# Kernel optimization log

Hardware: AMD Instinct MI355X
Metric: run time of the kernel (lower is better)

Reference implementation:

```python
import jax, jax.numpy as jnp
import numpy as np

B, T, D, F, E = 2, 2048, 1024, 4096, 8
TOP_K = 2


def setup_inputs() -> dict:
    key = jax.random.key(0)
    k0, k1, k2, k3 = jax.random.split(key, 4)
    x = jax.random.normal(k0, (B, T, D), dtype=jnp.float32)
    Wr = jax.random.normal(k1, (D, E), dtype=jnp.float32) * 0.02   # router (no bias)
    W1 = jax.random.normal(k2, (E, D, F), dtype=jnp.float32) * 0.02
    b1 = jnp.zeros((E, F), dtype=jnp.float32)
    W2 = jax.random.normal(k3, (E, F, D), dtype=jnp.float32) * 0.02
    b2 = jnp.zeros((E, D), dtype=jnp.float32)
    return {"x": x, "Wr": Wr, "W1": W1, "b1": b1, "W2": W2, "b2": b2}


def reference(x, Wr, W1, b1, W2, b2):
    # Router: softmax over experts, top-k select, renormalize selected probs.
    logits = jnp.einsum('btd,de->bte', x, Wr)                      # [B,T,E]
    probs = jax.nn.softmax(logits, axis=-1)
    top_v, top_i = jax.lax.top_k(probs, TOP_K)                     # [B,T,K]
    top_v = top_v / jnp.sum(top_v, axis=-1, keepdims=True)
    # Combine weights: scatter renormalized top-k probs back to expert slots.
    combine = jnp.sum(jax.nn.one_hot(top_i, E, dtype=x.dtype) * top_v[..., None], axis=-2)  # [B,T,E]
    # Expert FFNs (Linear -> exact GELU -> Linear); dropout inactive at eval.
    h = jax.nn.gelu(jnp.einsum('btd,edf->ebtf', x, W1) + b1[:, None, None, :],
                    approximate=False)                              # [E,B,T,F]
    y = jnp.einsum('ebtf,efd->ebtd', h, W2) + b2[:, None, None, :]  # [E,B,T,D]
    # Weighted sum over selected experts (combine is zero for unselected).
    out = jnp.einsum('ebtd,bte->btd', y, combine)
    return out
```

## Files before the change

### kernel.cpp

```cpp
#include <hip/hip_runtime.h>
#include <hip/hip_bf16.h>
#include <math.h>

#define B_  2
#define T_  2048
#define D_  1024
#define F_  4096
#define E_  8
#define NTOK 4096
#define TOPK 2
#define NROW 8192

typedef unsigned short bf16_t;
typedef float f32x4 __attribute__((ext_vector_type(4)));
typedef int   i32x4 __attribute__((ext_vector_type(4)));

#define OFF_CNT   0
#define OFF_BASE  32
#define OFF_TIDX  64
#define OFF_TW    32832
#define OFF_LIST  65600
#define OFF_WGT   196672
#define OFF_H_OLD 327744
#define WS_OLD    (OFF_H_OLD + (size_t)NROW * F_ * 2)
#define OFF_SLOT  327744
#define OFF_XB    (1u << 20)
#define OFF_W1T   (OFF_XB  + (size_t)NTOK * D_ * 2)
#define OFF_W2T   (OFF_W1T + (size_t)E_ * F_ * D_ * 2)
#define OFF_HN    (OFF_W2T + (size_t)E_ * D_ * F_ * 2)
#define OFF_Y     (OFF_HN  + (size_t)NROW * F_ * 2)
#define WS_MFMA   (OFF_Y   + (size_t)NROW * D_ * 4)

__device__ __forceinline__ float gelu_exact(float v) {
    return 0.5f * v * (1.0f + erff(v * 0.70710678118654752440f));
}

__device__ __forceinline__ unsigned short f2bf_rne(float f) {
    union { float f; unsigned int u; } v; v.f = f;
    unsigned int r = (v.u + 0x7fffu + ((v.u >> 16) & 1u)) >> 16;
    return (unsigned short)r;
}

__device__ __forceinline__ float bf2f(unsigned int u) {
    union { unsigned int i; float f; } v; v.i = u << 16; return v.f;
}

__device__ __forceinline__ void gld16(const void* g, void* l) {
    __builtin_amdgcn_global_load_lds(
        (const __attribute__((address_space(1))) unsigned int*)g,
        (__attribute__((address_space(3))) unsigned int*)l, 16, 0, 0);
}

__device__ __forceinline__ void mfma16(const i32x4& a, const i32x4& b, f32x4& c) {
    asm("v_mfma_f32_16x16x32_bf16 %0, %1, %2, %0" : "+v"(c) : "v"(a), "v"(b));
}

__global__ __launch_bounds__(64) void router_kernel(
    const float* __restrict__ x, const float* __restrict__ Wr,
    int* __restrict__ top_idx, float* __restrict__ top_w,
    int* __restrict__ cnt, int* __restrict__ list, float* __restrict__ wgt,
    int* __restrict__ slot, int mode)
{
    const int n = blockIdx.x;
    const int lane = threadIdx.x;
    const float* xr = x + (size_t)n * D_;

    float acc[E_];
#pragma unroll
    for (int e = 0; e < E_; ++e) acc[e] = 0.f;

    for (int d = lane; d < D_; d += 64) {
        const float xv = xr[d];
#pragma unroll
        for (int e = 0; e < E_; ++e)
            acc[e] += xv * Wr[d * E_ + e];
    }
#pragma unroll
    for (int e = 0; e < E_; ++e) {
        float v = acc[e];
#pragma unroll
        for (int off = 32; off > 0; off >>= 1)
            v += __shfl_down(v, off, 64);
        acc[e] = v;
    }
    if (lane == 0) {
        float m = acc[0];
#pragma unroll
        for (int e = 1; e < E_; ++e) m = fmaxf(m, acc[e]);
        float p[E_];
#pragma unroll
        for (int e = 0; e < E_; ++e) p[e] = __expf(acc[e] - m);
        int i0 = 0; float v0 = p[0];
#pragma unroll
        for (int e = 1; e < E_; ++e) if (p[e] > v0) { v0 = p[e]; i0 = e; }
        int i1 = (i0 == 0) ? 1 : 0; float v1 = p[i1];
#pragma unroll
        for (int e = 0; e < E_; ++e) {
            if (e == i0) continue;
            if (p[e] > v1) { v1 = p[e]; i1 = e; }
        }
        const float inv = 1.f / (v0 + v1);
        const float w0 = v0 * inv, w1 = v1 * inv;
        top_idx[n * TOPK + 0] = i0;
        top_idx[n * TOPK + 1] = i1;
        top_w[n * TOPK + 0] = w0;
        top_w[n * TOPK + 1] = w1;
        if (mode & 1) {
            int p0 = atomicAdd(&cnt[i0], 1);
            list[i0 * NTOK + p0] = n;  wgt[i0 * NTOK + p0] = w0;
            int p1 = atomicAdd(&cnt[i1], 1);
            list[i1 * NTOK + p1] = n;  wgt[i1 * NTOK + p1] = w1;
            if (mode & 2) {
                slot[n * TOPK + 0] = (i0 << 16) | p0;
                slot[n * TOPK + 1] = (i1 << 16) | p1;
            }
        }
    }
}

__global__ void prefix_kernel(const int* __restrict__ cnt, int* __restrict__ base)
{
    if (threadIdx.x == 0 && blockIdx.x == 0) {
        int s = 0;
#pragma unroll
        for (int e = 0; e < E_; ++e) { base[e] = s; s += cnt[e]; }
    }
}

__global__ __launch_bounds__(256) void convert_x_kernel(
    const float* __restrict__ x, bf16_t* __restrict__ xb)
{
    const int i = blockIdx.x * 256 + threadIdx.x;
    const float4 v = ((const float4*)x)[i];
    uint2 o;
    o.x = (unsigned int)f2bf_rne(v.x) | ((unsigned int)f2bf_rne(v.y) << 16);
    o.y = (unsigned int)f2bf_rne(v.z) | ((unsigned int)f2bf_rne(v.w) << 16);
    ((uint2*)xb)[i] = o;
}

__global__ __launch_bounds__(256) void transpose_kernel(
    const float* __restrict__ src, bf16_t* __restrict__ dst, int R, int C)
{
    __shared__ float tile[64][65];
    const int z  = blockIdx.z;
    const int r0 = blockIdx.y * 64;
    const int c0 = blockIdx.x * 64;
    const float* s = src + (size_t)z * R * C;
    bf16_t*      d = dst + (size_t)z * R * C;
    const int tx = threadIdx.x & 63;
    const int ty = threadIdx.x >> 6;
#pragma unroll
    for (int i = 0; i < 16; ++i) {
        const int r = i * 4 + ty;
        tile[r][tx] = s[(size_t)(r0 + r) * C + c0 + tx];
    }
    __syncthreads();
#pragma unroll
    for (int i = 0; i < 16; ++i) {
        const int c = i * 4 + ty;
        d[(size_t)(c0 + c) * R + r0 + tx] = f2bf_rne(tile[tx][c]);
    }
}

__global__ __launch_bounds__(256) void mgemm1_kernel(
    const bf16_t* __restrict__ Xb, const bf16_t* __restrict__ W1T,
    const float* __restrict__ b1,
    const int* __restrict__ cnt, const int* __restrict__ base,
    const int* __restrict__ list, bf16_t* __restrict__ H)
{
    __shared__ __align__(16) bf16_t As[128 * 32];
    __shared__ __align__(16) bf16_t Bs[128 * 32];

    const int e  = blockIdx.z;
    const int ce = cnt[e];
    const int m0 = blockIdx.y * 128;
    if (m0 >= ce) return;
    const int n0 = blockIdx.x * 128;
    const int be = base[e];
    const int tid  = threadIdx.x;
    const int lane = tid & 63, wave = tid >> 6;
    const int wr = wave >> 1, wc = wave & 1;
    const int quad = lane >> 4, l16 = lane & 15;

    const int mA = tid >> 2, cA = tid & 3;
    int r0i = m0 + mA;        if (r0i >= ce) r0i = ce - 1;
    int r1i = m0 + mA + 64;   if (r1i >= ce) r1i = ce - 1;
    const bf16_t* gA0 = Xb + (size_t)list[e * NTOK + r0i] * D_ + cA * 8;
    const bf16_t* gA1 = Xb + (size_t)list[e * NTOK + r1i] * D_ + cA * 8;
    const bf16_t* W1Te = W1T + (size_t)e * F_ * D_;
    const bf16_t* gB0 = W1Te + (size_t)(n0 + mA) * D_ + cA * 8;
    const bf16_t* gB1 = W1Te + (size_t)(n0 + mA + 64) * D_ + cA * 8;
    bf16_t* lA = As + wave * 512;
    bf16_t* lB = Bs + wave * 512;

    f32x4 acc[4][4] = {};

    for (int k0 = 0; k0 < D_; k0 += 32) {
        gld16(gA0 + k0, lA);
        gld16(gA1 + k0, lA + 2048);
        gld16(gB0 + k0, lB);
        gld16(gB1 + k0, lB + 2048);
        __syncthreads();
        i32x4 af[4], bfv[4];
#pragma unroll
        for (int i = 0; i < 4; ++i) {
            af[i]  = *(const i32x4*)(As + (wr * 64 + i * 16 + l16) * 32 + quad * 8);
            bfv[i] = *(const i32x4*)(Bs + (wc * 64 + i * 16 + l16) * 32 + quad * 8);
        }
#pragma unroll
        for (int i = 0; i < 4; ++i)
#pragma unroll
            for (int j = 0; j < 4; ++j)
                mfma16(af[i], bfv[j], acc[i][j]);
        __syncthreads();
    }
    asm volatile("s_nop 7\n\ts_nop 7");

    const float* b1e = b1 + (size_t)e * F_;
#pragma unroll
    for (int i = 0; i < 4; ++i) {
        const int rl = wr * 64 + i * 16 + quad * 4;
#pragma unroll
        for (int j = 0; j < 4; ++j) {
            const int col = n0 + wc * 64 + j * 16 + l16;
            const float bb = b1e[col];
#pragma unroll
            for (int r = 0; r < 4; ++r) {
                const int p = m0 + rl + r;
                if (p < ce)
                    H[(size_t)(be + p) * F_ + col] = f2bf_rne(gelu_exact(acc[i][j][r] + bb));
            }
        }
    }
}

__global__ __launch_bounds__(256) void mgemm2_kernel(
    const bf16_t* __restrict__ H, const bf16_t* __restrict__ W2T,
    const float* __restrict__ b2,
    const int* __restrict__ cnt, const int* __restrict__ base,
    float* __restrict__ Y)
{
    __shared__ __align__(16) bf16_t As[128 * 32];
    __shared__ __align__(16) bf16_t Bs[128 * 32];

    const int e  = blockIdx.z;
    const int ce = cnt[e];
    const int m0 = blockIdx.y * 128;
    if (m0 >= ce) return;
    const int n0 = blockIdx.x * 128;
    const int be = base[e];
    const int tid  = threadIdx.x;
    const int lane = tid & 63, wave = tid >> 6;
    const int wr = wave >> 1, wc = wave & 1;
    const int quad = lane >> 4, l16 = lane & 15;

    const int mA = tid >> 2, cA = tid & 3;
    int r0i = m0 + mA;        if (r0i >= ce) r0i = ce - 1;
    int r1i = m0 + mA + 64;   if (r1i >= ce) r1i = ce - 1;
    const bf16_t* gA0 = H + (size_t)(be + r0i) * F_ + cA * 8;
    const bf16_t* gA1 = H + (size_t)(be + r1i) * F_ + cA * 8;
    const bf16_t* W2Te = W2T + (size_t)e * D_ * F_;
    const bf16_t* gB0 = W2Te + (size_t)(n0 + mA) * F_ + cA * 8;
    const bf16_t* gB1 = W2Te + (size_t)(n0 + mA + 64) * F_ + cA * 8;
    bf16_t* lA = As + wave * 512;
    bf16_t* lB = Bs + wave * 512;

    f32x4 acc[4][4] = {};

    for (int k0 = 0; k0 < F_; k0 += 32) {
        gld16(gA0 + k0, lA);
        gld16(gA1 + k0, lA + 2048);
        gld16(gB0 + k0, lB);
        gld16(gB1 + k0, lB + 2048);
        __syncthreads();
        i32x4 af[4], bfv[4];
#pragma unroll
        for (int i = 0; i < 4; ++i) {
            af[i]  = *(const i32x4*)(As + (wr * 64 + i * 16 + l16) * 32 + quad * 8);
            bfv[i] = *(const i32x4*)(Bs + (wc * 64 + i * 16 + l16) * 32 + quad * 8);
        }
#pragma unroll
        for (int i = 0; i < 4; ++i)
#pragma unroll
            for (int j = 0; j < 4; ++j)
                mfma16(af[i], bfv[j], acc[i][j]);
        __syncthreads();
    }
    asm volatile("s_nop 7\n\ts_nop 7");

    const float* b2e = b2 + (size_t)e * D_;
#pragma unroll
    for (int i = 0; i < 4; ++i) {
        const int rl = wr * 64 + i * 16 + quad * 4;
#pragma unroll
        for (int j = 0; j < 4; ++j) {
            const int col = n0 + wc * 64 + j * 16 + l16;
            const float bb = b2e[col];
#pragma unroll
            for (int r = 0; r < 4; ++r) {
                const int p = m0 + rl + r;
                if (p < ce)
                    Y[(size_t)(be + p) * D_ + col] = acc[i][j][r] + bb;
            }
        }
    }
}

__global__ __launch_bounds__(256) void combine_kernel(
    const float* __restrict__ Y, const int* __restrict__ slot,
    const float* __restrict__ tw, const int* __restrict__ base,
    float* __restrict__ out)
{
    const int n = blockIdx.x;
    const int t = threadIdx.x;
    const int s0 = slot[n * TOPK + 0], s1 = slot[n * TOPK + 1];
    const float w0 = tw[n * TOPK + 0], w1 = tw[n * TOPK + 1];
    const int r0 = base[s0 >> 16] + (s0 & 0xffff);
    const int r1 = base[s1 >> 16] + (s1 & 0xffff);
    const float4 y0 = ((const float4*)(Y + (size_t)r0 * D_))[t];
    const float4 y1 = ((const float4*)(Y + (size_t)r1 * D_))[t];
    float4 o;
    o.x = w0 * y0.x + w1 * y1.x;
    o.y = w0 * y0.y + w1 * y1.y;
    o.z = w0 * y0.z + w1 * y1.z;
    o.w = w0 * y0.w + w1 * y1.w;
    ((float4*)(out + (size_t)n * D_))[t] = o;
}

#define BM 128
#define BN 128
#define BK 16

__global__ __launch_bounds__(256) void gemm1_kernel(
    const float* __restrict__ x, const float* __restrict__ W1,
    const float* __restrict__ b1,
    const int* __restrict__ cnt, const int* __restrict__ base,
    const int* __restrict__ list, bf16_t* __restrict__ H)
{
    __shared__ __align__(16) float Xs[BK][BM + 4];
    __shared__ __align__(16) float Ws[BK][BN + 4];

    const int e  = blockIdx.z;
    const int ce = cnt[e];
    const int m0 = blockIdx.y * BM;
    if (m0 >= ce) return;
    const int n0 = blockIdx.x * BN;
    const int be = base[e];
    const int t  = threadIdx.x;
    const int tx = t & 15, ty = t >> 4;

    const int xr_row = t >> 1;
    const int xr_c0  = (t & 1) * 8;
    const int p_x    = m0 + xr_row;
    const float* xrow = (p_x < ce) ? (x + (size_t)list[e * NTOK + p_x] * D_) : nullptr;
    const int wr_kk = t >> 4;
    const int wr_c0 = (t & 15) * 8;
    const float* W1e = W1 + (size_t)e * D_ * F_;

    float acc[8][8];
#pragma unroll
    for (int i = 0; i < 8; ++i)
#pragma unroll
        for (int j = 0; j < 8; ++j) acc[i][j] = 0.f;

    for (int k0 = 0; k0 < D_; k0 += BK) {
        float xv[8];
        if (xrow) {
            const float4 a = *(const float4*)(xrow + k0 + xr_c0);
            const float4 b = *(const float4*)(xrow + k0 + xr_c0 + 4);
            xv[0]=a.x; xv[1]=a.y; xv[2]=a.z; xv[3]=a.w;
            xv[4]=b.x; xv[5]=b.y; xv[6]=b.z; xv[7]=b.w;
        } else {
#pragma unroll
            for (int j = 0; j < 8; ++j) xv[j] = 0.f;
        }
#pragma unroll
        for (int j = 0; j < 8; ++j) Xs[xr_c0 + j][xr_row] = xv[j];
        {
            const float* wr = W1e + (size_t)(k0 + wr_kk) * F_ + (n0 + wr_c0);
            *(float4*)&Ws[wr_kk][wr_c0]     = *(const float4*)(wr);
            *(float4*)&Ws[wr_kk][wr_c0 + 4] = *(const float4*)(wr + 4);
        }
        __syncthreads();
#pragma unroll 4
        for (int kk = 0; kk < BK; ++kk) {
            float a[8], b[8];
            *(float4*)&a[0] = *(const float4*)&Xs[kk][ty * 8];
            *(float4*)&a[4] = *(const float4*)&Xs[kk][ty * 8 + 4];
            *(float4*)&b[0] = *(const float4*)&Ws[kk][tx * 8];
            *(float4*)&b[4] = *(const float4*)&Ws[kk][tx * 8 + 4];
#pragma unroll
            for (int i = 0; i < 8; ++i)
#pragma unroll
                for (int j = 0; j < 8; ++j)
                    acc[i][j] += a[i] * b[j];
        }
        __syncthreads();
    }

    const float* b1e = b1 + (size_t)e * F_;
    float bb[8];
#pragma unroll
    for (int j = 0; j < 8; ++j) bb[j] = b1e[n0 + tx * 8 + j];
#pragma unroll
    for (int i = 0; i < 8; ++i) {
        const int p = m0 + ty * 8 + i;
        if (p >= ce) continue;
        unsigned int pk[4];
#pragma unroll
        for (int jj = 0; jj < 4; ++jj) {
            const float g0 = gelu_exact(acc[i][2 * jj]     + bb[2 * jj]);
            const float g1 = gelu_exact(acc[i][2 * jj + 1] + bb[2 * jj + 1]);
            pk[jj] = (unsigned int)f2bf_rne(g0) | ((unsigned int)f2bf_rne(g1) << 16);
        }
        uint4 v; v.x = pk[0]; v.y = pk[1]; v.z = pk[2]; v.w = pk[3];
        *(uint4*)(H + (size_t)(be + p) * F_ + n0 + tx * 8) = v;
    }
}

__global__ __launch_bounds__(256) void gemm2_kernel(
    const bf16_t* __restrict__ H, const float* __restrict__ W2,
    const float* __restrict__ b2,
    const int* __restrict__ cnt, const int* __restrict__ base,
    const int* __restrict__ list, const float* __restrict__ wgt,
    float* __restrict__ out)
{
    __shared__ __align__(16) float Hs[BK][BM + 4];
    __shared__ __align__(16) float Ws[BK][BN + 4];

    const int e  = blockIdx.z;
    const int ce = cnt[e];
    const int m0 = blockIdx.y * BM;
    if (m0 >= ce) return;
    const int n0 = blockIdx.x * BN;
    const int be = base[e];
    const int t  = threadIdx.x;
    const int tx = t & 15, ty = t >> 4;

    const int hr_row = t >> 1;
    const int hr_c0  = (t & 1) * 8;
    const int p_h    = m0 + hr_row;
    const bf16_t* hrow = (p_h < ce) ? (H + (size_t)(be + p_h) * F_) : nullptr;
    const int wr_kk = t >> 4;
    const int wr_c0 = (t & 15) * 8;
    const float* W2e = W2 + (size_t)e * F_ * D_;

    float acc[8][8];
#pragma unroll
    for (int i = 0; i < 8; ++i)
#pragma unroll
        for (int j = 0; j < 8; ++j) acc[i][j] = 0.f;

    for (int k0 = 0; k0 < F_; k0 += BK) {
        float hv[8];
        if (hrow) {
            const uint4 u = *(const uint4*)(hrow + k0 + hr_c0);
            hv[0] = bf2f(u.x & 0xffffu); hv[1] = bf2f(u.x >> 16);
            hv[2] = bf2f(u.y & 0xffffu); hv[3] = bf2f(u.y >> 16);
            hv[4] = bf2f(u.z & 0xffffu); hv[5] = bf2f(u.z >> 16);
            hv[6] = bf2f(u.w & 0xffffu); hv[7] = bf2f(u.w >> 16);
        } else {
#pragma unroll
            for (int j = 0; j < 8; ++j) hv[j] = 0.f;
        }
#pragma unroll
        for (int j = 0; j < 8; ++j) Hs[hr_c0 + j][hr_row] = hv[j];
        {
            const float* wr = W2e + (size_t)(k0 + wr_kk) * D_ + (n0 + wr_c0);
            *(float4*)&Ws[wr_kk][wr_c0]     = *(const float4*)(wr);
            *(float4*)&Ws[wr_kk][wr_c0 + 4] = *(const float4*)(wr + 4);
        }
        __syncthreads();
#pragma unroll 4
        for (int kk = 0; kk < BK; ++kk) {
            float a[8], b[8];
            *(float4*)&a[0] = *(const float4*)&Hs[kk][ty * 8];
            *(float4*)&a[4] = *(const float4*)&Hs[kk][ty * 8 + 4];
            *(float4*)&b[0] = *(const float4*)&Ws[kk][tx * 8];
            *(float4*)&b[4] = *(const float4*)&Ws[kk][tx * 8 + 4];
#pragma unroll
            for (int i = 0; i < 8; ++i)
#pragma unroll
                for (int j = 0; j < 8; ++j)
                    acc[i][j] += a[i] * b[j];
        }
        __syncthreads();
    }

    const float* b2e = b2 + (size_t)e * D_;
    float bb[8];
#pragma unroll
    for (int j = 0; j < 8; ++j) bb[j] = b2e[n0 + tx * 8 + j];
#pragma unroll
    for (int i = 0; i < 8; ++i) {
        const int p = m0 + ty * 8 + i;
        if (p >= ce) continue;
        const int   n = list[e * NTOK + p];
        const float w = wgt[e * NTOK + p];
        float* op = out + (size_t)n * D_ + n0 + tx * 8;
#pragma unroll
        for (int j = 0; j < 8; ++j)
            atomicAdd(&op[j], w * (acc[i][j] + bb[j]));
    }
}

__global__ __launch_bounds__(256) void fallback_expert_kernel(
    const float* __restrict__ x,
    const float* __restrict__ W1, const float* __restrict__ b1,
    const float* __restrict__ W2, const float* __restrict__ b2,
    const int* __restrict__ top_idx, const float* __restrict__ top_w,
    float* __restrict__ out)
{
    __shared__ float x_lds[D_];
    __shared__ float h_lds[F_];

    const int n = blockIdx.x;
    const int t = threadIdx.x;

    ((float4*)x_lds)[t] = ((const float4*)(x + (size_t)n * D_))[t];
    __syncthreads();

    const int d0 = t * 4;
    float acc_out[4] = {0.f, 0.f, 0.f, 0.f};

    for (int k = 0; k < TOPK; ++k) {
        const int   e = top_idx[n * TOPK + k];
        const float w = top_w[n * TOPK + k];
        const float* W1e = W1 + (size_t)e * D_ * F_;
        const float* b1e = b1 + (size_t)e * F_;
#pragma unroll
        for (int tile = 0; tile < 2; ++tile) {
            const int base_f = tile * 2048 + t * 8;
            float a[8];
#pragma unroll
            for (int j = 0; j < 8; ++j) a[j] = b1e[base_f + j];
            const float4* wp = (const float4*)(W1e + base_f);
            for (int d = 0; d < D_; ++d) {
                const float4 w0 = wp[(size_t)d * (F_ / 4)];
                const float4 w1 = wp[(size_t)d * (F_ / 4) + 1];
                const float xv = x_lds[d];
                a[0] += xv * w0.x; a[1] += xv * w0.y;
                a[2] += xv * w0.z; a[3] += xv * w0.w;
                a[4] += xv * w1.x; a[5] += xv * w1.y;
                a[6] += xv * w1.z; a[7] += xv * w1.w;
            }
#pragma unroll
            for (int j = 0; j < 8; ++j)
                h_lds[base_f + j] = gelu_exact(a[j]);
        }
        __syncthreads();

        const float* W2e = W2 + (size_t)e * F_ * D_;
        const float* b2e = b2 + (size_t)e * D_;
        float y[4];
#pragma unroll
        for (int j = 0; j < 4; ++j) y[j] = b2e[d0 + j];
        const float4* wp2 = (const float4*)(W2e + d0);
        for (int f = 0; f < F_; ++f) {
            const float4 wv = wp2[(size_t)f * (D_ / 4)];
            const float hv = h_lds[f];
            y[0] += hv * wv.x; y[1] += hv * wv.y;
            y[2] += hv * wv.z; y[3] += hv * wv.w;
        }
#pragma unroll
        for (int j = 0; j < 4; ++j) acc_out[j] += w * y[j];
        __syncthreads();
    }

    float4 o; o.x = acc_out[0]; o.y = acc_out[1]; o.z = acc_out[2]; o.w = acc_out[3];
    *(float4*)(out + (size_t)n * D_ + d0) = o;
}

extern "C" void kernel_launch(void* const* d_in, const int* in_sizes, int n_in,
                              void* d_out, int out_size, void* d_ws, size_t ws_size,
                              hipStream_t stream) {
    const float* x  = (const float*)d_in[0];
    const float* Wr = (const float*)d_in[1];
    const float* W1 = (const float*)d_in[2];
    const float* b1 = (const float*)d_in[3];
    const float* W2 = (const float*)d_in[4];
    const float* b2 = (const float*)d_in[5];
    float* out = (float*)d_out;

    char* ws = (char*)d_ws;
    int*    cnt   = (int*)(ws + OFF_CNT);
    int*    basep = (int*)(ws + OFF_BASE);
    int*    tidx  = (int*)(ws + OFF_TIDX);
    float*  tw    = (float*)(ws + OFF_TW);
    int*    list  = (int*)(ws + OFF_LIST);
    float*  wgt   = (float*)(ws + OFF_WGT);

    if (ws_size >= WS_MFMA) {
        int*    slot = (int*)(ws + OFF_SLOT);
        bf16_t* Xb   = (bf16_t*)(ws + OFF_XB);
        bf16_t* W1T  = (bf16_t*)(ws + OFF_W1T);
        bf16_t* W2T  = (bf16_t*)(ws + OFF_W2T);
        bf16_t* H    = (bf16_t*)(ws + OFF_HN);
        float*  Y    = (float*)(ws + OFF_Y);

        hipMemsetAsync(cnt, 0, E_ * sizeof(int), stream);
        router_kernel<<<NTOK, 64, 0, stream>>>(x, Wr, tidx, tw, cnt, list, wgt, slot, 3);
        prefix_kernel<<<1, 64, 0, stream>>>(cnt, basep);
        convert_x_kernel<<<NTOK * D_ / 4 / 256, 256, 0, stream>>>(x, Xb);
        transpose_kernel<<<dim3(F_ / 64, D_ / 64, E_), 256, 0, stream>>>(W1, W1T, D_, F_);
        transpose_kernel<<<dim3(D_ / 64, F_ / 64, E_), 256, 0, stream>>>(W2, W2T, F_, D_);
        mgemm1_kernel<<<dim3(F_ / 128, NTOK / 128, E_), 256, 0, stream>>>(
            Xb, W1T, b1, cnt, basep, list, H);
        mgemm2_kernel<<<dim3(D_ / 128, NTOK / 128, E_), 256, 0, stream>>>(
            H, W2T, b2, cnt, basep, Y);
        combine_kernel<<<NTOK, 256, 0, stream>>>(Y, slot, tw, basep, out);
    } else if (ws_size >= WS_OLD) {
        bf16_t* H = (bf16_t*)(ws + OFF_H_OLD);
        hipMemsetAsync(cnt, 0, E_ * sizeof(int), stream);
        router_kernel<<<NTOK, 64, 0, stream>>>(x, Wr, tidx, tw, cnt, list, wgt, nullptr, 1);
        prefix_kernel<<<1, 64, 0, stream>>>(cnt, basep);
        hipMemsetAsync(out, 0, (size_t)NTOK * D_ * sizeof(float), stream);
        gemm1_kernel<<<dim3(F_ / BN, NTOK / BM, E_), 256, 0, stream>>>(
            x, W1, b1, cnt, basep, list, H);
        gemm2_kernel<<<dim3(D_ / BN, NTOK / BM, E_), 256, 0, stream>>>(
            H, W2, b2, cnt, basep, list, wgt, out);
    } else {
        router_kernel<<<NTOK, 64, 0, stream>>>(x, Wr, tidx, tw, cnt, list, wgt, nullptr, 0);
        fallback_expert_kernel<<<NTOK, 256, 0, stream>>>(
            x, W1, b1, W2, b2, tidx, tw, out);
    }
}
```

Before: 728.1 us.

## Double-buffer LDS in expert GEMMs, split-K second GEMM, vectorize transpose stores

Both grouped expert GEMMs now use two LDS buffers and issue the next K-tile's global-to-LDS loads before computing the current one, removing one barrier per iteration and overlapping loads with MFMA work. When the workspace is large enough, the second GEMM splits K into two slabs that write separate partial Y buffers, and the combine kernel sums them; this doubles the grid to fill more CUs at the cost of extra Y traffic. The weight transpose kernel now packs four bf16 values per 8-byte store instead of writing scalar 2-byte stores.

```diff
diff --git a/kernel.cpp b/kernel.cpp
--- a/kernel.cpp
+++ b/kernel.cpp
@@ -29,7 +29,8 @@
 #define OFF_W2T   (OFF_W1T + (size_t)E_ * F_ * D_ * 2)
 #define OFF_HN    (OFF_W2T + (size_t)E_ * D_ * F_ * 2)
 #define OFF_Y     (OFF_HN  + (size_t)NROW * F_ * 2)
-#define WS_MFMA   (OFF_Y   + (size_t)NROW * D_ * 4)
+#define WS_MFMA   (OFF_Y + (size_t)NROW * D_ * 4)
+#define WS_MFMA2  (OFF_Y + 2 * (size_t)NROW * D_ * 4)
 
 __device__ __forceinline__ float gelu_exact(float v) {
     return 0.5f * v * (1.0f + erff(v * 0.70710678118654752440f));
@@ -155,10 +156,15 @@
         tile[r][tx] = s[(size_t)(r0 + r) * C + c0 + tx];
     }
     __syncthreads();
-#pragma unroll
-    for (int i = 0; i < 16; ++i) {
-        const int c = i * 4 + ty;
-        d[(size_t)(c0 + c) * R + r0 + tx] = f2bf_rne(tile[tx][c]);
+    const int rc = (threadIdx.x & 15) * 4;
+    const int cc = threadIdx.x >> 4;
+#pragma unroll
+    for (int i = 0; i < 4; ++i) {
+        const int c = i * 16 + cc;
+        uint2 o;
+        o.x = (unsigned int)f2bf_rne(tile[rc    ][c]) | ((unsigned int)f2bf_rne(tile[rc + 1][c]) << 16);
+        o.y = (unsigned int)f2bf_rne(tile[rc + 2][c]) | ((unsigned int)f2bf_rne(tile[rc + 3][c]) << 16);
+        *(uint2*)(d + (size_t)(c0 + c) * R + r0 + rc) = o;
     }
 }
 
@@ -168,8 +174,8 @@
     const int* __restrict__ cnt, const int* __restrict__ base,
     const int* __restrict__ list, bf16_t* __restrict__ H)
 {
-    __shared__ __align__(16) bf16_t As[128 * 32];
-    __shared__ __align__(16) bf16_t Bs[128 * 32];
+    __shared__ __align__(16) bf16_t As[2][128 * 32];
+    __shared__ __align__(16) bf16_t Bs[2][128 * 32];
 
     const int e  = blockIdx.z;
     const int ce = cnt[e];
@@ -190,30 +196,34 @@
     const bf16_t* W1Te = W1T + (size_t)e * F_ * D_;
     const bf16_t* gB0 = W1Te + (size_t)(n0 + mA) * D_ + cA * 8;
     const bf16_t* gB1 = W1Te + (size_t)(n0 + mA + 64) * D_ + cA * 8;
-    bf16_t* lA = As + wave * 512;
-    bf16_t* lB = Bs + wave * 512;
 
     f32x4 acc[4][4] = {};
 
+#define PREF1(bufi, kk) do { \
+        gld16(gA0 + (kk), As[bufi] + wave * 512); \
+        gld16(gA1 + (kk), As[bufi] + 2048 + wave * 512); \
+        gld16(gB0 + (kk), Bs[bufi] + wave * 512); \
+        gld16(gB1 + (kk), Bs[bufi] + 2048 + wave * 512); } while (0)
+
+    PREF1(0, 0);
+    int buf = 0;
     for (int k0 = 0; k0 < D_; k0 += 32) {
-        gld16(gA0 + k0, lA);
-        gld16(gA1 + k0, lA + 2048);
-        gld16(gB0 + k0, lB);
-        gld16(gB1 + k0, lB + 2048);
-        __syncthreads();
+        __syncthreads();
+        if (k0 + 32 < D_) PREF1(buf ^ 1, k0 + 32);
         i32x4 af[4], bfv[4];
 #pragma unroll
         for (int i = 0; i < 4; ++i) {
-            af[i]  = *(const i32x4*)(As + (wr * 64 + i * 16 + l16) * 32 + quad * 8);
-            bfv[i] = *(const i32x4*)(Bs + (wc * 64 + i * 16 + l16) * 32 + quad * 8);
+            af[i]  = *(const i32x4*)(As[buf] + (wr * 64 + i * 16 + l16) * 32 + quad * 8);
+            bfv[i] = *(const i32x4*)(Bs[buf] + (wc * 64 + i * 16 + l16) * 32 + quad * 8);
         }
 #pragma unroll
         for (int i = 0; i < 4; ++i)
 #pragma unroll
             for (int j = 0; j < 4; ++j)
                 mfma16(af[i], bfv[j], acc[i][j]);
-        __syncthreads();
-    }
+        buf ^= 1;
+    }
+#undef PREF1
     asm volatile("s_nop 7\n\ts_nop 7");
 
     const float* b1e = b1 + (size_t)e * F_;
@@ -240,13 +250,17 @@
     const int* __restrict__ cnt, const int* __restrict__ base,
     float* __restrict__ Y)
 {
-    __shared__ __align__(16) bf16_t As[128 * 32];
-    __shared__ __align__(16) bf16_t Bs[128 * 32];
-
-    const int e  = blockIdx.z;
+    __shared__ __align__(16) bf16_t As[2][128 * 32];
+    __shared__ __align__(16) bf16_t Bs[2][128 * 32];
+
+    const int kslabs = gridDim.z / E_;
+    const int e  = blockIdx.z % E_;
+    const int s  = blockIdx.z / E_;
     const int ce = cnt[e];
     const int m0 = blockIdx.y * 128;
     if (m0 >= ce) return;
+    const int klen  = F_ / kslabs;
+    const int kbase = s * klen;
     const int n0 = blockIdx.x * 128;
     const int be = base[e];
     const int tid  = threadIdx.x;
@@ -257,37 +271,42 @@
     const int mA = tid >> 2, cA = tid & 3;
     int r0i = m0 + mA;        if (r0i >= ce) r0i = ce - 1;
     int r1i = m0 + mA + 64;   if (r1i >= ce) r1i = ce - 1;
-    const bf16_t* gA0 = H + (size_t)(be + r0i) * F_ + cA * 8;
-    const bf16_t* gA1 = H + (size_t)(be + r1i) * F_ + cA * 8;
+    const bf16_t* gA0 = H + (size_t)(be + r0i) * F_ + cA * 8 + kbase;
+    const bf16_t* gA1 = H + (size_t)(be + r1i) * F_ + cA * 8 + kbase;
     const bf16_t* W2Te = W2T + (size_t)e * D_ * F_;
-    const bf16_t* gB0 = W2Te + (size_t)(n0 + mA) * F_ + cA * 8;
-    const bf16_t* gB1 = W2Te + (size_t)(n0 + mA + 64) * F_ + cA * 8;
-    bf16_t* lA = As + wave * 512;
-    bf16_t* lB = Bs + wave * 512;
+    const bf16_t* gB0 = W2Te + (size_t)(n0 + mA) * F_ + cA * 8 + kbase;
+    const bf16_t* gB1 = W2Te + (size_t)(n0 + mA + 64) * F_ + cA * 8 + kbase;
 
     f32x4 acc[4][4] = {};
 
-    for (int k0 = 0; k0 < F_; k0 += 32) {
-        gld16(gA0 + k0, lA);
-        gld16(gA1 + k0, lA + 2048);
-        gld16(gB0 + k0, lB);
-        gld16(gB1 + k0, lB + 2048);
-        __syncthreads();
+#define PREF2(bufi, kk) do { \
+        gld16(gA0 + (kk), As[bufi] + wave * 512); \
+        gld16(gA1 + (kk), As[bufi] + 2048 + wave * 512); \
+        gld16(gB0 + (kk), Bs[bufi] + wave * 512); \
+        gld16(gB1 + (kk), Bs[bufi] + 2048 + wave * 512); } while (0)
+
+    PREF2(0, 0);
+    int buf = 0;
+    for (int k0 = 0; k0 < klen; k0 += 32) {
+        __syncthreads();
+        if (k0 + 32 < klen) PREF2(buf ^ 1, k0 + 32);
         i32x4 af[4], bfv[4];
 #pragma unroll
         for (int i = 0; i < 4; ++i) {
-            af[i]  = *(const i32x4*)(As + (wr * 64 + i * 16 + l16) * 32 + quad * 8);
-            bfv[i] = *(const i32x4*)(Bs + (wc * 64 + i * 16 + l16) * 32 + quad * 8);
+            af[i]  = *(const i32x4*)(As[buf] + (wr * 64 + i * 16 + l16) * 32 + quad * 8);
+            bfv[i] = *(const i32x4*)(Bs[buf] + (wc * 64 + i * 16 + l16) * 32 + quad * 8);
         }
 #pragma unroll
         for (int i = 0; i < 4; ++i)
 #pragma unroll
             for (int j = 0; j < 4; ++j)
                 mfma16(af[i], bfv[j], acc[i][j]);
-        __syncthreads();
-    }
+        buf ^= 1;
+    }
+#undef PREF2
     asm volatile("s_nop 7\n\ts_nop 7");
 
+    float* Ys = Y + (size_t)s * NROW * D_;
     const float* b2e = b2 + (size_t)e * D_;
 #pragma unroll
     for (int i = 0; i < 4; ++i) {
@@ -295,12 +314,12 @@
 #pragma unroll
         for (int j = 0; j < 4; ++j) {
             const int col = n0 + wc * 64 + j * 16 + l16;
-            const float bb = b2e[col];
+            const float bb = (s == 0) ? b2e[col] : 0.f;
 #pragma unroll
             for (int r = 0; r < 4; ++r) {
                 const int p = m0 + rl + r;
                 if (p < ce)
-                    Y[(size_t)(be + p) * D_ + col] = acc[i][j][r] + bb;
+                    Ys[(size_t)(be + p) * D_ + col] = acc[i][j][r] + bb;
             }
         }
     }
@@ -309,7 +328,7 @@
 __global__ __launch_bounds__(256) void combine_kernel(
     const float* __restrict__ Y, const int* __restrict__ slot,
     const float* __restrict__ tw, const int* __restrict__ base,
-    float* __restrict__ out)
+    float* __restrict__ out, int kslabs)
 {
     const int n = blockIdx.x;
     const int t = threadIdx.x;
@@ -317,8 +336,15 @@
     const float w0 = tw[n * TOPK + 0], w1 = tw[n * TOPK + 1];
     const int r0 = base[s0 >> 16] + (s0 & 0xffff);
     const int r1 = base[s1 >> 16] + (s1 & 0xffff);
-    const float4 y0 = ((const float4*)(Y + (size_t)r0 * D_))[t];
-    const float4 y1 = ((const float4*)(Y + (size_t)r1 * D_))[t];
+    float4 y0 = ((const float4*)(Y + (size_t)r0 * D_))[t];
+    float4 y1 = ((const float4*)(Y + (size_t)r1 * D_))[t];
+    if (kslabs == 2) {
+        const float* Y1 = Y + (size_t)NROW * D_;
+        const float4 a = ((const float4*)(Y1 + (size_t)r0 * D_))[t];
+        const float4 b = ((const float4*)(Y1 + (size_t)r1 * D_))[t];
+        y0.x += a.x; y0.y += a.y; y0.z += a.z; y0.w += a.w;
+        y1.x += b.x; y1.y += b.y; y1.z += b.z; y1.w += b.w;
+    }
     float4 o;
     o.x = w0 * y0.x + w1 * y1.x;
     o.y = w0 * y0.y + w1 * y1.y;
@@ -591,6 +617,7 @@
     float*  wgt   = (float*)(ws + OFF_WGT);
 
     if (ws_size >= WS_MFMA) {
+        const int kslabs = (ws_size >= WS_MFMA2) ? 2 : 1;
         int*    slot = (int*)(ws + OFF_SLOT);
         bf16_t* Xb   = (bf16_t*)(ws + OFF_XB);
         bf16_t* W1T  = (bf16_t*)(ws + OFF_W1T);
@@ -606,9 +633,9 @@
         transpose_kernel<<<dim3(D_ / 64, F_ / 64, E_), 256, 0, stream>>>(W2, W2T, F_, D_);
         mgemm1_kernel<<<dim3(F_ / 128, NTOK / 128, E_), 256, 0, stream>>>(
             Xb, W1T, b1, cnt, basep, list, H);
-        mgemm2_kernel<<<dim3(D_ / 128, NTOK / 128, E_), 256, 0, stream>>>(
+        mgemm2_kernel<<<dim3(D_ / 128, NTOK / 128, E_ * kslabs), 256, 0, stream>>>(
             H, W2T, b2, cnt, basep, Y);
-        combine_kernel<<<NTOK, 256, 0, stream>>>(Y, slot, tw, basep, out);
+        combine_kernel<<<NTOK, 256, 0, stream>>>(Y, slot, tw, basep, out, kslabs);
     } else if (ws_size >= WS_OLD) {
         bf16_t* H = (bf16_t*)(ws + OFF_H_OLD);
         hipMemsetAsync(cnt, 0, E_ * sizeof(int), stream);
```

Result: faster. 711.1 us (-2.3%).
